# Performance work log

Measured on AMD Instinct MI355X. Metric: run time of the kernel, lower is better.

Reference implementation:

```python
import jax, jax.numpy as jnp
import numpy as np

B, S, IN, OUT, RANK, LORA_R = 2, 2048, 4096, 4096, 8, 16
LORA_SCALING = 16.0 / LORA_R  # alpha / r = 1.0


def setup_inputs() -> dict:
    key = jax.random.key(0)
    ks = jax.random.split(key, 6)
    x = jax.random.normal(ks[0], (B, S, IN), dtype=jnp.float32)
    weight = jax.random.normal(ks[1], (OUT, IN), dtype=jnp.float32) * 0.02  # Q (snapped weights)
    scale_A = jax.random.normal(ks[2], (OUT, RANK), dtype=jnp.float32) * 0.1
    scale_B = jax.random.normal(ks[3], (RANK, IN), dtype=jnp.float32) * 0.1
    rank_magnitude = jnp.ones((RANK,), dtype=jnp.float32)
    lora_A = jax.random.normal(ks[4], (LORA_R, IN), dtype=jnp.float32) * 0.02
    lora_B = jax.random.normal(ks[5], (OUT, LORA_R), dtype=jnp.float32) * 0.02
    return {"x": x, "weight": weight, "scale_A": scale_A, "scale_B": scale_B,
            "rank_magnitude": rank_magnitude, "lora_A": lora_A, "lora_B": lora_B}


def reference(x, weight, scale_A, scale_B, rank_magnitude, lora_A, lora_B):
    # y_o = sum_k g_k * a_{ok} * sum_i Q_{oi} * b_{ki} * x_i
    #     = sum_i (Q_{oi} * sum_k (g_k a_{ok}) b_{ki}) x_i
    # i.e. a single dense GEMM with the precomputed effective weight
    # W_eff = Q * ((scale_A * g) @ scale_B)  -- same math, rank dim folded once.
    S_mat = jnp.einsum('ok,ki->oi', scale_A * rank_magnitude[None, :], scale_B)  # [out, in]
    W_eff = weight * S_mat                                                        # [out, in]
    y = jnp.einsum('bsi,oi->bso', x, W_eff)                                       # [B, S, out]
    # LoRA add: (x @ A^T) @ B^T * scaling
    y = y + ((x @ lora_A.T) @ lora_B.T) * LORA_SCALING
    return y
```

## Files before the change

kernel.cpp:

```cpp
#include <hip/hip_runtime.h>

#define M_DIM 4096
#define IN_DIM 4096
#define OUT_DIM 4096
#define RANK 8
#define LORA_R 16
#define LORA_SCALING 1.0f

typedef __bf16 bf16;
typedef bf16  bf16x4 __attribute__((ext_vector_type(4)));
typedef bf16  bf16x8 __attribute__((ext_vector_type(8)));
typedef float f32x4  __attribute__((ext_vector_type(4)));
typedef float f32x16 __attribute__((ext_vector_type(16)));

#define OG 8
__global__ __launch_bounds__(256) void prep_fused(
    const float* __restrict__ weight, const float* __restrict__ scale_A,
    const float* __restrict__ scale_B, const float* __restrict__ g,
    const float* __restrict__ lora_A, const float* __restrict__ lora_B,
    const float* __restrict__ x, bf16* __restrict__ wt, bf16* __restrict__ xb)
{
    const int t = threadIdx.x;
    if (blockIdx.x < 2048) {
        __shared__ float s_sa[OG][RANK];
        __shared__ float s_lb[OG][LORA_R];
        const int o0 = (blockIdx.x >> 2) * OG;
        if (t < OG * RANK) {
            int r8 = t / RANK, k = t % RANK;
            s_sa[r8][k] = scale_A[(o0 + r8) * RANK + k] * g[k];
        }
        if (t < OG * LORA_R) {
            int r8 = t / LORA_R, r = t % LORA_R;
            s_lb[r8][r] = lora_B[(o0 + r8) * LORA_R + r] * LORA_SCALING;
        }
        __syncthreads();

        const int i0 = ((blockIdx.x & 3) * 256 + t) * 4;

        f32x4 acc[OG];
#pragma unroll
        for (int r8 = 0; r8 < OG; ++r8) acc[r8] = {0.f, 0.f, 0.f, 0.f};
#pragma unroll
        for (int k = 0; k < RANK; ++k) {
            f32x4 sbk = *(const f32x4*)(scale_B + k * IN_DIM + i0);
#pragma unroll
            for (int r8 = 0; r8 < OG; ++r8) acc[r8] += s_sa[r8][k] * sbk;
        }
#pragma unroll
        for (int r8 = 0; r8 < OG; ++r8) {
            f32x4 wv = *(const f32x4*)(weight + (size_t)(o0 + r8) * IN_DIM + i0);
            acc[r8] *= wv;
        }
#pragma unroll
        for (int r = 0; r < LORA_R; ++r) {
            f32x4 lak = *(const f32x4*)(lora_A + r * IN_DIM + i0);
#pragma unroll
            for (int r8 = 0; r8 < OG; ++r8) acc[r8] += s_lb[r8][r] * lak;
        }
#pragma unroll
        for (int r8 = 0; r8 < OG; ++r8) {
            bf16x4 h = { (bf16)acc[r8][0], (bf16)acc[r8][1],
                         (bf16)acc[r8][2], (bf16)acc[r8][3] };
            *(bf16x4*)(wt + (size_t)(o0 + r8) * IN_DIM + i0) = h;
        }
    } else {
        const int n4  = (M_DIM * IN_DIM) / 4;
        int idx    = (blockIdx.x - 2048) * 256 + t;
        int stride = 2048 * 256;
        for (int i = idx; i < n4; i += stride) {
            f32x4 v = *(const f32x4*)(x + (size_t)i * 4);
            bf16x4 h = { (bf16)v[0], (bf16)v[1], (bf16)v[2], (bf16)v[3] };
            *(bf16x4*)(xb + (size_t)i * 4) = h;
        }
    }
}

#define BM 256
#define BN 256
#define BK 64

__device__ __forceinline__ void gload16(const bf16* g, bf16* l) {
    __builtin_amdgcn_global_load_lds(
        (const __attribute__((address_space(1))) void*)g,
        (__attribute__((address_space(3))) void*)l,
        16, 0, 0);
}

#define MFMA(d, a, b) d = __builtin_amdgcn_mfma_f32_32x32x16_bf16((a), (b), (d), 0, 0, 0)
#define BARRIER() __builtin_amdgcn_s_barrier()
#define WAIT_LGKM0() asm volatile("s_waitcnt lgkmcnt(0)" ::: "memory")
#define WAIT_VM(n)   asm volatile("s_waitcnt vmcnt(" #n ")" ::: "memory")

__global__ __launch_bounds__(512, 2) void gemm_bt(
    const bf16* __restrict__ A,
    const bf16* __restrict__ Bw,
    float* __restrict__ C)
{
    __shared__ __align__(16) char smem[131072];

    const int t  = threadIdx.x;
    const int w  = t >> 6;
    const int l  = t & 63;
    const int lh = l >> 5;
    const int ln = l & 31;
    const int wm = w >> 2;
    const int wn = w & 3;

    const int bid = blockIdx.x;
    const int xcd = bid & 7;
    const int loc = bid >> 3;
    const int mt  = (xcd & 3) * 4 + (loc >> 3);
    const int nt  = (xcd >> 2) * 8 + (loc & 7);
    const int m0  = mt * BM;
    const int n0  = nt * BN;

    const int srow   = l >> 2;
    const int schunk = (l & 3) ^ ((l >> 3) & 3);
    const size_t soff = (size_t)(w * 16 + srow) * IN_DIM + schunk * 8;
    const bf16* gA = A  + (size_t)m0 * IN_DIM + soff;
    const bf16* gB = Bw + (size_t)n0 * IN_DIM + soff;
    const int wA = w << 10;

#define STAGE(gsrc, dstbyte) do {                                   \
        bf16* d_ = (bf16*)(smem + (dstbyte));                       \
        gload16((gsrc), d_);                                        \
        gload16((gsrc) + (size_t)128 * IN_DIM, d_ + 4096);          \
    } while (0)

    const int s4  = (ln >> 1) & 3;
    const int cEv = ((lh)     ^ s4) << 4;
    const int cOd = ((2 + lh) ^ s4) << 4;
    const char* aB0 = smem + (wm * 128 + ln) * 64;
    const char* bB0 = smem + 65536 + (wn * 64 + ln) * 64;

    f32x16 acc[4][2] = {};

    STAGE(gA + 0,  0      + wA);
    STAGE(gB + 0,  65536  + wA);
    STAGE(gA + 32, 16384  + wA);
    STAGE(gB + 32, 65536 + 16384 + wA);
    STAGE(gA + 64, 32768  + wA);
    STAGE(gB + 64, 65536 + 32768 + wA);
    WAIT_VM(4);
    BARRIER();

#pragma unroll 2
    for (int kt = 0; kt < 64; ++kt) {
        const int p   = kt & 1;
        const int po  = p << 15;
        const int qo  = po ^ 32768;
        const int kc1 = (kt + 1 < 64) ? (kt + 1) * BK : 0;
        const int kc2 = (kt + 2 < 64) ? (kt + 2) * BK : 0;

        bf16x8 a00 = *(const bf16x8*)(aB0 + po + cEv);
        bf16x8 a01 = *(const bf16x8*)(aB0 + po + cOd);
        bf16x8 a10 = *(const bf16x8*)(aB0 + po + 2048 + cEv);
        bf16x8 a11 = *(const bf16x8*)(aB0 + po + 2048 + cOd);
        bf16x8 b00 = *(const bf16x8*)(bB0 + po + cEv);
        bf16x8 b01 = *(const bf16x8*)(bB0 + po + cOd);
        bf16x8 b10 = *(const bf16x8*)(bB0 + po + 2048 + cEv);
        bf16x8 b11 = *(const bf16x8*)(bB0 + po + 2048 + cOd);
        STAGE(gA + kc1 + 32, qo + 16384 + wA);
        BARRIER();
        WAIT_LGKM0();
        __builtin_amdgcn_s_setprio(1);
        MFMA(acc[0][0], a00, b00); MFMA(acc[0][1], a00, b10);
        MFMA(acc[1][0], a10, b00); MFMA(acc[1][1], a10, b10);
        MFMA(acc[0][0], a01, b01); MFMA(acc[0][1], a01, b11);
        MFMA(acc[1][0], a11, b01); MFMA(acc[1][1], a11, b11);
        __builtin_amdgcn_s_setprio(0);
        BARRIER();

        bf16x8 a20 = *(const bf16x8*)(aB0 + po + 4096 + cEv);
        bf16x8 a21 = *(const bf16x8*)(aB0 + po + 4096 + cOd);
        bf16x8 a30 = *(const bf16x8*)(aB0 + po + 6144 + cEv);
        bf16x8 a31 = *(const bf16x8*)(aB0 + po + 6144 + cOd);
        STAGE(gB + kc1 + 32, 65536 + qo + 16384 + wA);
        BARRIER();
        WAIT_LGKM0();
        __builtin_amdgcn_s_setprio(1);
        MFMA(acc[2][0], a20, b00); MFMA(acc[2][1], a20, b10);
        MFMA(acc[3][0], a30, b00); MFMA(acc[3][1], a30, b10);
        MFMA(acc[2][0], a21, b01); MFMA(acc[2][1], a21, b11);
        MFMA(acc[3][0], a31, b01); MFMA(acc[3][1], a31, b11);
        __builtin_amdgcn_s_setprio(0);
        BARRIER();

        a00 = *(const bf16x8*)(aB0 + po + 16384 + cEv);
        a01 = *(const bf16x8*)(aB0 + po + 16384 + cOd);
        a10 = *(const bf16x8*)(aB0 + po + 16384 + 2048 + cEv);
        a11 = *(const bf16x8*)(aB0 + po + 16384 + 2048 + cOd);
        b00 = *(const bf16x8*)(bB0 + po + 16384 + cEv);
        b01 = *(const bf16x8*)(bB0 + po + 16384 + cOd);
        b10 = *(const bf16x8*)(bB0 + po + 16384 + 2048 + cEv);
        b11 = *(const bf16x8*)(bB0 + po + 16384 + 2048 + cOd);
        STAGE(gA + kc2, po + wA);
        BARRIER();
        WAIT_LGKM0();
        __builtin_amdgcn_s_setprio(1);
        MFMA(acc[0][0], a00, b00); MFMA(acc[0][1], a00, b10);
        MFMA(acc[1][0], a10, b00); MFMA(acc[1][1], a10, b10);
        MFMA(acc[0][0], a01, b01); MFMA(acc[0][1], a01, b11);
        MFMA(acc[1][0], a11, b01); MFMA(acc[1][1], a11, b11);
        __builtin_amdgcn_s_setprio(0);
        BARRIER();

        a20 = *(const bf16x8*)(aB0 + po + 16384 + 4096 + cEv);
        a21 = *(const bf16x8*)(aB0 + po + 16384 + 4096 + cOd);
        a30 = *(const bf16x8*)(aB0 + po + 16384 + 6144 + cEv);
        a31 = *(const bf16x8*)(aB0 + po + 16384 + 6144 + cOd);
        STAGE(gB + kc2, 65536 + po + wA);
        BARRIER();
        WAIT_LGKM0();
        __builtin_amdgcn_s_setprio(1);
        MFMA(acc[2][0], a20, b00); MFMA(acc[2][1], a20, b10);
        MFMA(acc[3][0], a30, b00); MFMA(acc[3][1], a30, b10);
        MFMA(acc[2][0], a21, b01); MFMA(acc[2][1], a21, b11);
        MFMA(acc[3][0], a31, b01); MFMA(acc[3][1], a31, b11);
        __builtin_amdgcn_s_setprio(0);
        WAIT_VM(4);
        BARRIER();
    }

    asm volatile("s_waitcnt vmcnt(0) lgkmcnt(0)" ::: "memory");
    BARRIER();
    float* sEw = (float*)(void*)smem + w * (32 * 33);
#pragma unroll
    for (int tm2 = 0; tm2 < 4; ++tm2)
#pragma unroll
        for (int tn2 = 0; tn2 < 2; ++tn2) {
#pragma unroll
            for (int j = 0; j < 16; ++j) {
                int row = (j & 3) + 8 * (j >> 2) + 4 * lh;
                sEw[row * 33 + ln] = acc[tm2][tn2][j];
            }
#pragma unroll
            for (int q = 0; q < 4; ++q) {
                int r4 = q * 8 + (l >> 3);
                int c4 = (l & 7) * 4;
                f32x4 v = { sEw[r4 * 33 + c4],     sEw[r4 * 33 + c4 + 1],
                            sEw[r4 * 33 + c4 + 2], sEw[r4 * 33 + c4 + 3] };
                *(f32x4*)(C + (size_t)(m0 + wm * 128 + tm2 * 32 + r4) * OUT_DIM
                            + (n0 + wn * 64 + tn2 * 32 + c4)) = v;
            }
        }
}

extern "C" void kernel_launch(void* const* d_in, const int* in_sizes, int n_in,
                              void* d_out, int out_size, void* d_ws, size_t ws_size,
                              hipStream_t stream) {
    (void)in_sizes; (void)n_in; (void)out_size; (void)ws_size;
    const float* x        = (const float*)d_in[0];
    const float* weight   = (const float*)d_in[1];
    const float* scale_A  = (const float*)d_in[2];
    const float* scale_B  = (const float*)d_in[3];
    const float* g        = (const float*)d_in[4];
    const float* lora_A   = (const float*)d_in[5];
    const float* lora_B   = (const float*)d_in[6];
    float* out = (float*)d_out;

    bf16* xb = (bf16*)d_ws;
    bf16* wt = (bf16*)((char*)d_ws + (size_t)M_DIM * IN_DIM * sizeof(bf16));

    prep_fused<<<4096, 256, 0, stream>>>(weight, scale_A, scale_B, g,
                                         lora_A, lora_B, x, wt, xb);

    gemm_bt<<<(M_DIM / BM) * (OUT_DIM / BN), 512, 0, stream>>>(xb, wt, out);
}
```

Measured before the change: 307.8 us.

## Restructure GEMM into quadrant schedule with 16x16x32 MFMA and full-K-tile double buffering

Measured after the change: 301.3 us. -2.1%, faster.

```diff
diff --git a/kernel.cpp b/kernel.cpp
--- a/kernel.cpp
+++ b/kernel.cpp
@@ -11,7 +11,6 @@
 typedef bf16  bf16x4 __attribute__((ext_vector_type(4)));
 typedef bf16  bf16x8 __attribute__((ext_vector_type(8)));
 typedef float f32x4  __attribute__((ext_vector_type(4)));
-typedef float f32x16 __attribute__((ext_vector_type(16)));
 
 #define OG 8
 __global__ __launch_bounds__(256) void prep_fused(
@@ -86,10 +85,38 @@
         16, 0, 0);
 }
 
-#define MFMA(d, a, b) d = __builtin_amdgcn_mfma_f32_32x32x16_bf16((a), (b), (d), 0, 0, 0)
-#define BARRIER() __builtin_amdgcn_s_barrier()
+#define BARRIER()    __builtin_amdgcn_s_barrier()
 #define WAIT_LGKM0() asm volatile("s_waitcnt lgkmcnt(0)" ::: "memory")
 #define WAIT_VM(n)   asm volatile("s_waitcnt vmcnt(" #n ")" ::: "memory")
+
+__device__ __forceinline__ void load_af(bf16x8 (&aF)[4][2], const char* aB, int off) {
+#pragma unroll
+    for (int r = 0; r < 4; ++r)
+#pragma unroll
+        for (int ks = 0; ks < 2; ++ks)
+            aF[r][ks] = *(const bf16x8*)(aB + off + r * 2048 + ks * 64);
+}
+__device__ __forceinline__ void load_bf(bf16x8 (&bF)[2][2], const char* bB, int off) {
+#pragma unroll
+    for (int n = 0; n < 2; ++n)
+#pragma unroll
+        for (int ks = 0; ks < 2; ++ks)
+            bF[n][ks] = *(const bf16x8*)(bB + off + n * 2048 + ks * 64);
+}
+
+template<int QM, int QN>
+__device__ __forceinline__ void mfma_quad(f32x4 (&acc)[2][2][4][2],
+                                          const bf16x8 (&aF)[4][2],
+                                          const bf16x8 (&bF)[2][2]) {
+#pragma unroll
+    for (int ks = 0; ks < 2; ++ks)
+#pragma unroll
+        for (int r = 0; r < 4; ++r)
+#pragma unroll
+            for (int n = 0; n < 2; ++n)
+                acc[QM][QN][r][n] = __builtin_amdgcn_mfma_f32_16x16x32_bf16(
+                    aF[r][ks], bF[n][ks], acc[QM][QN][r][n], 0, 0, 0);
+}
 
 __global__ __launch_bounds__(512, 2) void gemm_bt(
     const bf16* __restrict__ A,
@@ -101,8 +128,6 @@
     const int t  = threadIdx.x;
     const int w  = t >> 6;
     const int l  = t & 63;
-    const int lh = l >> 5;
-    const int ln = l & 31;
     const int wm = w >> 2;
     const int wn = w & 3;
 
@@ -114,109 +139,76 @@
     const int m0  = mt * BM;
     const int n0  = nt * BN;
 
-    const int srow   = l >> 2;
-    const int schunk = (l & 3) ^ ((l >> 3) & 3);
-    const size_t soff = (size_t)(w * 16 + srow) * IN_DIM + schunk * 8;
-    const bf16* gA = A  + (size_t)m0 * IN_DIM + soff;
-    const bf16* gB = Bw + (size_t)n0 * IN_DIM + soff;
-    const int wA = w << 10;
-
-#define STAGE(gsrc, dstbyte) do {                                   \
-        bf16* d_ = (bf16*)(smem + (dstbyte));                       \
-        gload16((gsrc), d_);                                        \
-        gload16((gsrc) + (size_t)128 * IN_DIM, d_ + 4096);          \
+    const int scol = 8 * ((l & 7) ^ (((l >> 5) & 1) << 1));
+    const bf16* gAs = A  + (size_t)(m0 + w * 8 + (l >> 3)) * IN_DIM + scol;
+    const bf16* gBs = Bw + (size_t)(n0 + w * 8 + (l >> 3)) * IN_DIM + scol;
+
+#define STAGEH(gbase, kc, dstOff) do {                                        \
+        gload16((gbase) + (kc),                                               \
+                (bf16*)(smem + (dstOff) + (w << 10)));                        \
+        gload16((gbase) + (kc) + (size_t)64 * IN_DIM,                         \
+                (bf16*)(smem + (dstOff) + 8192 + (w << 10)));                 \
     } while (0)
 
-    const int s4  = (ln >> 1) & 3;
-    const int cEv = ((lh)     ^ s4) << 4;
-    const int cOd = ((2 + lh) ^ s4) << 4;
-    const char* aB0 = smem + (wm * 128 + ln) * 64;
-    const char* bB0 = smem + 65536 + (wn * 64 + ln) * 64;
-
-    f32x16 acc[4][2] = {};
-
-    STAGE(gA + 0,  0      + wA);
-    STAGE(gB + 0,  65536  + wA);
-    STAGE(gA + 32, 16384  + wA);
-    STAGE(gB + 32, 65536 + 16384 + wA);
-    STAGE(gA + 64, 32768  + wA);
-    STAGE(gB + 64, 65536 + 32768 + wA);
+    const int fr  = l & 15;
+    const int sw2 = ((l >> 2) & 1) << 1;
+    const int sl0 = (((l >> 4) & 3) ^ sw2) << 4;
+    const char* aB = smem + wm * 8192 + fr * 128 + sl0;
+    const char* bB = smem + 32768 + wn * 4096 + fr * 128 + sl0;
+
+    f32x4 acc[2][2][4][2] = {};
+    bf16x8 aF[4][2], bF[2][2];
+
+    STAGEH(gAs, 0, 0);
+    STAGEH(gBs, 0, 32768);
+    STAGEH(gBs + (size_t)128 * IN_DIM, 0, 49152);
+    STAGEH(gAs + (size_t)128 * IN_DIM, 0, 16384);
     WAIT_VM(4);
     BARRIER();
 
 #pragma unroll 2
     for (int kt = 0; kt < 64; ++kt) {
-        const int p   = kt & 1;
-        const int po  = p << 15;
-        const int qo  = po ^ 32768;
-        const int kc1 = (kt + 1 < 64) ? (kt + 1) * BK : 0;
-        const int kc2 = (kt + 2 < 64) ? (kt + 2) * BK : 0;
-
-        bf16x8 a00 = *(const bf16x8*)(aB0 + po + cEv);
-        bf16x8 a01 = *(const bf16x8*)(aB0 + po + cOd);
-        bf16x8 a10 = *(const bf16x8*)(aB0 + po + 2048 + cEv);
-        bf16x8 a11 = *(const bf16x8*)(aB0 + po + 2048 + cOd);
-        bf16x8 b00 = *(const bf16x8*)(bB0 + po + cEv);
-        bf16x8 b01 = *(const bf16x8*)(bB0 + po + cOd);
-        bf16x8 b10 = *(const bf16x8*)(bB0 + po + 2048 + cEv);
-        bf16x8 b11 = *(const bf16x8*)(bB0 + po + 2048 + cOd);
-        STAGE(gA + kc1 + 32, qo + 16384 + wA);
-        BARRIER();
-        WAIT_LGKM0();
-        __builtin_amdgcn_s_setprio(1);
-        MFMA(acc[0][0], a00, b00); MFMA(acc[0][1], a00, b10);
-        MFMA(acc[1][0], a10, b00); MFMA(acc[1][1], a10, b10);
-        MFMA(acc[0][0], a01, b01); MFMA(acc[0][1], a01, b11);
-        MFMA(acc[1][0], a11, b01); MFMA(acc[1][1], a11, b11);
-        __builtin_amdgcn_s_setprio(0);
-        BARRIER();
-
-        bf16x8 a20 = *(const bf16x8*)(aB0 + po + 4096 + cEv);
-        bf16x8 a21 = *(const bf16x8*)(aB0 + po + 4096 + cOd);
-        bf16x8 a30 = *(const bf16x8*)(aB0 + po + 6144 + cEv);
-        bf16x8 a31 = *(const bf16x8*)(aB0 + po + 6144 + cOd);
-        STAGE(gB + kc1 + 32, 65536 + qo + 16384 + wA);
-        BARRIER();
-        WAIT_LGKM0();
-        __builtin_amdgcn_s_setprio(1);
-        MFMA(acc[2][0], a20, b00); MFMA(acc[2][1], a20, b10);
-        MFMA(acc[3][0], a30, b00); MFMA(acc[3][1], a30, b10);
-        MFMA(acc[2][0], a21, b01); MFMA(acc[2][1], a21, b11);
-        MFMA(acc[3][0], a31, b01); MFMA(acc[3][1], a31, b11);
-        __builtin_amdgcn_s_setprio(0);
-        BARRIER();
-
-        a00 = *(const bf16x8*)(aB0 + po + 16384 + cEv);
-        a01 = *(const bf16x8*)(aB0 + po + 16384 + cOd);
-        a10 = *(const bf16x8*)(aB0 + po + 16384 + 2048 + cEv);
-        a11 = *(const bf16x8*)(aB0 + po + 16384 + 2048 + cOd);
-        b00 = *(const bf16x8*)(bB0 + po + 16384 + cEv);
-        b01 = *(const bf16x8*)(bB0 + po + 16384 + cOd);
-        b10 = *(const bf16x8*)(bB0 + po + 16384 + 2048 + cEv);
-        b11 = *(const bf16x8*)(bB0 + po + 16384 + 2048 + cOd);
-        STAGE(gA + kc2, po + wA);
-        BARRIER();
-        WAIT_LGKM0();
-        __builtin_amdgcn_s_setprio(1);
-        MFMA(acc[0][0], a00, b00); MFMA(acc[0][1], a00, b10);
-        MFMA(acc[1][0], a10, b00); MFMA(acc[1][1], a10, b10);
-        MFMA(acc[0][0], a01, b01); MFMA(acc[0][1], a01, b11);
-        MFMA(acc[1][0], a11, b01); MFMA(acc[1][1], a11, b11);
-        __builtin_amdgcn_s_setprio(0);
-        BARRIER();
-
-        a20 = *(const bf16x8*)(aB0 + po + 16384 + 4096 + cEv);
-        a21 = *(const bf16x8*)(aB0 + po + 16384 + 4096 + cOd);
-        a30 = *(const bf16x8*)(aB0 + po + 16384 + 6144 + cEv);
-        a31 = *(const bf16x8*)(aB0 + po + 16384 + 6144 + cOd);
-        STAGE(gB + kc2, 65536 + po + wA);
-        BARRIER();
-        WAIT_LGKM0();
-        __builtin_amdgcn_s_setprio(1);
-        MFMA(acc[2][0], a20, b00); MFMA(acc[2][1], a20, b10);
-        MFMA(acc[3][0], a30, b00); MFMA(acc[3][1], a30, b10);
-        MFMA(acc[2][0], a21, b01); MFMA(acc[2][1], a21, b11);
-        MFMA(acc[3][0], a31, b01); MFMA(acc[3][1], a31, b11);
+        const int po  = (kt & 1) << 16;
+        const int qo  = po ^ 65536;
+        const int kcn = (kt + 1 < 64) ? (kt + 1) * BK : 0;
+
+        load_af(aF, aB, po);
+        load_bf(bF, bB, po);
+        STAGEH(gAs, kcn, qo);
+        BARRIER();
+        WAIT_LGKM0();
+        __builtin_amdgcn_s_setprio(1);
+        mfma_quad<0, 0>(acc, aF, bF);
+        __builtin_amdgcn_s_setprio(0);
+        WAIT_VM(4);
+        BARRIER();
+
+        load_bf(bF, bB, po + 16384);
+        STAGEH(gBs, kcn, qo + 32768);
+        BARRIER();
+        WAIT_LGKM0();
+        __builtin_amdgcn_s_setprio(1);
+        mfma_quad<0, 1>(acc, aF, bF);
+        __builtin_amdgcn_s_setprio(0);
+        WAIT_VM(4);
+        BARRIER();
+
+        load_af(aF, aB, po + 16384);
+        STAGEH(gBs + (size_t)128 * IN_DIM, kcn, qo + 49152);
+        BARRIER();
+        WAIT_LGKM0();
+        __builtin_amdgcn_s_setprio(1);
+        mfma_quad<1, 1>(acc, aF, bF);
+        __builtin_amdgcn_s_setprio(0);
+        WAIT_VM(4);
+        BARRIER();
+
+        load_bf(bF, bB, po);
+        STAGEH(gAs + (size_t)128 * IN_DIM, kcn, qo + 16384);
+        BARRIER();
+        WAIT_LGKM0();
+        __builtin_amdgcn_s_setprio(1);
+        mfma_quad<1, 0>(acc, aF, bF);
         __builtin_amdgcn_s_setprio(0);
         WAIT_VM(4);
         BARRIER();
@@ -224,24 +216,29 @@
 
     asm volatile("s_waitcnt vmcnt(0) lgkmcnt(0)" ::: "memory");
     BARRIER();
-    float* sEw = (float*)(void*)smem + w * (32 * 33);
-#pragma unroll
-    for (int tm2 = 0; tm2 < 4; ++tm2)
-#pragma unroll
-        for (int tn2 = 0; tn2 < 2; ++tn2) {
-#pragma unroll
-            for (int j = 0; j < 16; ++j) {
-                int row = (j & 3) + 8 * (j >> 2) + 4 * lh;
-                sEw[row * 33 + ln] = acc[tm2][tn2][j];
-            }
-#pragma unroll
-            for (int q = 0; q < 4; ++q) {
-                int r4 = q * 8 + (l >> 3);
-                int c4 = (l & 7) * 4;
-                f32x4 v = { sEw[r4 * 33 + c4],     sEw[r4 * 33 + c4 + 1],
-                            sEw[r4 * 33 + c4 + 2], sEw[r4 * 33 + c4 + 3] };
-                *(f32x4*)(C + (size_t)(m0 + wm * 128 + tm2 * 32 + r4) * OUT_DIM
-                            + (n0 + wn * 64 + tn2 * 32 + c4)) = v;
+    float* sE = (float*)(void*)smem + w * (64 * 33);
+    const int er = l >> 4;
+    const int ec = l & 15;
+#pragma unroll
+    for (int QM = 0; QM < 2; ++QM)
+#pragma unroll
+        for (int QN = 0; QN < 2; ++QN) {
+#pragma unroll
+            for (int r = 0; r < 4; ++r)
+#pragma unroll
+                for (int n = 0; n < 2; ++n)
+#pragma unroll
+                    for (int j = 0; j < 4; ++j)
+                        sE[(r * 16 + er * 4 + j) * 33 + n * 16 + ec] =
+                            acc[QM][QN][r][n][j];
+#pragma unroll
+            for (int q = 0; q < 8; ++q) {
+                int r2 = q * 8 + (l >> 3);
+                int c2 = (l & 7) * 4;
+                f32x4 v = { sE[r2 * 33 + c2],     sE[r2 * 33 + c2 + 1],
+                            sE[r2 * 33 + c2 + 2], sE[r2 * 33 + c2 + 3] };
+                *(f32x4*)(C + (size_t)(m0 + QM * 128 + wm * 64 + r2) * OUT_DIM
+                            + (n0 + QN * 128 + wn * 32 + c2)) = v;
             }
         }
 }
```
